# Kernel optimization log

Measured on AMD Instinct MI355X. Metric: run time of the kernel, lower is better.

## Reference

```python
import jax, jax.numpy as jnp
import numpy as np

D_MODEL = 256
N_HEADS = 8
HEAD_DIM = D_MODEL // N_HEADS  # 32
N_LEVELS = 4
N_POINTS = 4
LEVEL_SHAPES = [(100, 100), (50, 50), (25, 25), (13, 13)]
LEVEL_STARTS = [0] + list(np.cumsum([h * w for h, w in LEVEL_SHAPES]))[:-1]
LEN_IN = int(sum(h * w for h, w in LEVEL_SHAPES))  # 13294
BATCH = 2
LEN_Q = LEN_IN  # encoder self-attention


def _offset_bias():
    # faithful to MSDeformAttn._reset_parameters for sampling_offsets bias
    thetas = np.arange(N_HEADS, dtype=np.float32) * (2.0 * np.pi / N_HEADS)
    grid = np.stack([np.cos(thetas), np.sin(thetas)], -1)
    grid = grid / np.abs(grid).max(-1, keepdims=True)
    grid = np.tile(grid.reshape(N_HEADS, 1, 1, 2), (1, N_LEVELS, N_POINTS, 1))
    for i in range(N_POINTS):
        grid[:, :, i, :] *= i + 1
    return jnp.asarray(grid.reshape(-1), dtype=jnp.float32)


def setup_inputs() -> dict:
    key = jax.random.key(0)
    ks = jax.random.split(key, 10)
    s = 1.0 / np.sqrt(D_MODEL)
    inp = {
        "query": jax.random.normal(ks[0], (BATCH, LEN_Q, D_MODEL), jnp.float32),
        "reference_points": jax.random.uniform(ks[1], (BATCH, LEN_Q, N_LEVELS, 2), jnp.float32),
        "input_flatten": jax.random.normal(ks[2], (BATCH, LEN_IN, D_MODEL), jnp.float32),
        "input_spatial_shapes": jnp.asarray(LEVEL_SHAPES, dtype=jnp.int32),
        "W_value": jax.random.normal(ks[3], (D_MODEL, D_MODEL), jnp.float32) * s,
        "b_value": jnp.zeros((D_MODEL,), jnp.float32),
        "W_off": jax.random.normal(ks[4], (D_MODEL, N_HEADS * N_LEVELS * N_POINTS * 2), jnp.float32) * 0.01,
        "b_off": _offset_bias(),
        "W_attn": jax.random.normal(ks[5], (D_MODEL, N_HEADS * N_LEVELS * N_POINTS), jnp.float32) * 0.01,
        "b_attn": jnp.zeros((N_HEADS * N_LEVELS * N_POINTS,), jnp.float32),
        "W_out": jax.random.normal(ks[6], (D_MODEL, D_MODEL), jnp.float32) * s,
        "b_out": jnp.zeros((D_MODEL,), jnp.float32),
    }
    return inp


def _corner(v_t, ix, iy, h, w):
    # v_t: (n, M, h*w, D); ix/iy: (n, M, LqP) int32. Zero padding outside.
    valid = (ix >= 0) & (ix < w) & (iy >= 0) & (iy < h)
    idx = jnp.clip(iy, 0, h - 1) * w + jnp.clip(ix, 0, w - 1)
    g = jnp.take_along_axis(v_t, idx[..., None], axis=2)  # (n, M, LqP, D)
    return g * valid[..., None].astype(v_t.dtype)


def _ms_deform_attn(query, reference_points, input_flatten,
                    W_value, b_value, W_off, b_off, W_attn, b_attn, W_out, b_out):
    n, lq, _ = query.shape
    value = (input_flatten @ W_value + b_value).reshape(n, LEN_IN, N_HEADS, HEAD_DIM)
    offs = (query @ W_off + b_off).reshape(n, lq, N_HEADS, N_LEVELS, N_POINTS, 2)
    aw = jax.nn.softmax(
        (query @ W_attn + b_attn).reshape(n, lq, N_HEADS, N_LEVELS * N_POINTS), axis=-1
    ).reshape(n, lq, N_HEADS, N_LEVELS, N_POINTS)
    # offset_normalizer = (w, h) per level
    norm = jnp.asarray([[w, h] for h, w in LEVEL_SHAPES], dtype=query.dtype)
    loc = reference_points[:, :, None, :, None, :] + offs / norm[None, None, None, :, None, :]

    acc = jnp.zeros((n, N_HEADS, lq, HEAD_DIM), dtype=value.dtype)
    for l, (h, w) in enumerate(LEVEL_SHAPES):
        s0 = LEVEL_STARTS[l]
        v_t = jnp.transpose(value[:, s0:s0 + h * w], (0, 2, 1, 3))  # (n, M, hw, D)
        ll = loc[:, :, :, l]  # (n, lq, M, P, 2) in [0,1]
        # grid_sample bilinear, align_corners=False: pixel = coord*size - 0.5
        x = ll[..., 0] * w - 0.5
        y = ll[..., 1] * h - 0.5
        x0 = jnp.floor(x); y0 = jnp.floor(y)
        tx = x - x0; ty = y - y0
        ix0 = x0.astype(jnp.int32); iy0 = y0.astype(jnp.int32)
        flat = lambda a: jnp.transpose(a, (0, 2, 1, 3)).reshape(n, N_HEADS, lq * N_POINTS)
        ix0f, iy0f = flat(ix0), flat(iy0)
        txf = flat(tx)[..., None]; tyf = flat(ty)[..., None]
        g00 = _corner(v_t, ix0f, iy0f, h, w)
        g01 = _corner(v_t, ix0f + 1, iy0f, h, w)
        g10 = _corner(v_t, ix0f, iy0f + 1, h, w)
        g11 = _corner(v_t, ix0f + 1, iy0f + 1, h, w)
        samp = (g00 * (1 - txf) * (1 - tyf) + g01 * txf * (1 - tyf)
                + g10 * (1 - txf) * tyf + g11 * txf * tyf)
        samp = samp.reshape(n, N_HEADS, lq, N_POINTS, HEAD_DIM)
        wl = jnp.transpose(aw[:, :, :, l], (0, 2, 1, 3))[..., None]  # (n, M, lq, P, 1)
        acc = acc + (samp * wl).sum(axis=3)

    out = jnp.transpose(acc, (0, 2, 1, 3)).reshape(n, lq, D_MODEL)
    return out @ W_out + b_out


def reference(query, reference_points, input_flatten, input_spatial_shapes,
              W_value, b_value, W_off, b_off, W_attn, b_attn, W_out, b_out):
    # input_spatial_shapes carried for signature fidelity; level geometry is static.
    return _ms_deform_attn(query, reference_points, input_flatten,
                           W_value, b_value, W_off, b_off, W_attn, b_attn, W_out, b_out)
```

## Files before the change

kernel.cpp:

```cpp
#include <hip/hip_runtime.h>

#define NH 8
#define HD 32
#define NL 4
#define NP 4
#define DM 256
#define LEN_IN_C 13294
#define LQ_C 13294
#define B_C 2
#define M_TOTAL (B_C * LQ_C)
#define MT_TILES 1662

typedef __attribute__((ext_vector_type(8))) short short8;
typedef __attribute__((ext_vector_type(4))) float floatx4;
typedef __attribute__((ext_vector_type(2))) float floatx2;

__device__ __forceinline__ unsigned short f2bf(float x) {
    union { float f; unsigned int u; } a; a.f = x;
    unsigned int r = (a.u + 0x7FFFu + ((a.u >> 16) & 1u)) >> 16;
    return (unsigned short)r;
}
__device__ __forceinline__ floatx2 up2(unsigned int u) {
    union { unsigned int u; float f; } lo, hi;
    lo.u = u << 16; hi.u = u & 0xffff0000u;
    floatx2 r; r.x = lo.f; r.y = hi.f; return r;
}
__device__ __forceinline__ unsigned int cvtpk_bf16(float lo, float hi) {
    unsigned int r;
    asm("v_cvt_pk_bf16_f32 %0, %1, %2" : "=v"(r) : "v"(lo), "v"(hi));
    return r;
}

__device__ __forceinline__ void conv_b_body(const float* __restrict__ W,
                                            unsigned short* __restrict__ Bsw,
                                            int Nsrc, int NTsrc, int NTtotal, int ntOff,
                                            int vblk) {
    const int u = vblk * 256 + threadIdx.x;
    const int lane = u & 63;
    const int unit = u >> 6;
    const int ntl = unit % NTsrc;
    const int kc = unit / NTsrc;
    const int n = ntl * 16 + (lane & 15);
    const int k0 = kc * 32 + (lane >> 4) * 8;
    short8 v;
#pragma unroll
    for (int j = 0; j < 8; ++j)
        v[j] = (short)f2bf(W[(size_t)(k0 + j) * Nsrc + n]);
    ((short8*)Bsw)[(size_t)(kc * NTtotal + ntOff + ntl) * 64 + lane] = v;
}

__global__ __launch_bounds__(256) void conv_weights_kernel(const float* __restrict__ Wv,
                                                           const float* __restrict__ Woff,
                                                           const float* __restrict__ Wattn,
                                                           const float* __restrict__ Wout,
                                                           const float* __restrict__ boff,
                                                           const float* __restrict__ battn,
                                                           unsigned short* __restrict__ BswV,
                                                           unsigned short* __restrict__ BswOA,
                                                           unsigned short* __restrict__ BswO,
                                                           float* __restrict__ fbias,
                                                           unsigned short* __restrict__ value,
                                                           unsigned short* __restrict__ AccSw) {
    const int blk = blockIdx.x;
    if (blk < 32)        conv_b_body(Wv,    BswV,  256, 16, 16, 0,  blk);
    else if (blk < 64)   conv_b_body(Woff,  BswOA, 256, 16, 24, 0,  blk - 32);
    else if (blk < 80)   conv_b_body(Wattn, BswOA, 128,  8, 24, 16, blk - 64);
    else if (blk < 112)  conv_b_body(Wout,  BswO,  256, 16, 16, 0,  blk - 80);
    else if (blk < 114) {
        const int t = (blk - 112) * 256 + threadIdx.x;
        if (t < 384) fbias[t] = (t < 256) ? boff[t] : battn[t - 256];
        else if (t < 416) {
            const int j = t - 384;
            value[-32 + j] = 0;
            value[(size_t)M_TOTAL * 256 + j] = 0;
        }
    } else {
        const int idx = threadIdx.x;
        if (idx < 128) {
            const int kc = idx >> 4;
            const int sub = idx & 15;
            const int lane = (12 + (sub & 3)) + 16 * (sub >> 2);
            const size_t unit = (size_t)(1661 * 8 + kc) * 64 + lane;
            short8 z = (short8){0, 0, 0, 0, 0, 0, 0, 0};
            ((short8*)AccSw)[unit] = z;
        }
    }
}

template <int NT, int OUTMODE>
__global__ __launch_bounds__(256) void mfma_gemm_f32a(const float* __restrict__ A,
                                                      const unsigned short* __restrict__ Bsw,
                                                      const float* __restrict__ bias,
                                                      void* __restrict__ Cout, int M) {
    constexpr int NTW = NT / 4;
    const int tid = threadIdx.x;
    const int lane = tid & 63;
    const int wave = tid >> 6;
    const int rt0 = blockIdx.x * 2;
    const int m = lane & 15;
    const int q = lane >> 4;

    const float* Ar0 = A + (size_t)min(rt0 * 16 + m, M - 1) * 256 + q * 8;
    const float* Ar1 = A + (size_t)min(rt0 * 16 + 16 + m, M - 1) * 256 + q * 8;
    const short8* Bu = (const short8*)Bsw;

    floatx4 acc[2][NTW];
#pragma unroll
    for (int r = 0; r < 2; ++r)
#pragma unroll
        for (int t = 0; t < NTW; ++t) acc[r][t] = (floatx4){0.f, 0.f, 0.f, 0.f};

#pragma unroll 2
    for (int kc = 0; kc < 8; ++kc) {
        const float4 f00 = *(const float4*)(Ar0 + kc * 32);
        const float4 f01 = *(const float4*)(Ar0 + kc * 32 + 4);
        const float4 f10 = *(const float4*)(Ar1 + kc * 32);
        const float4 f11 = *(const float4*)(Ar1 + kc * 32 + 4);
        union { uint4 u; short8 s; } c0, c1;
        c0.u.x = cvtpk_bf16(f00.x, f00.y); c0.u.y = cvtpk_bf16(f00.z, f00.w);
        c0.u.z = cvtpk_bf16(f01.x, f01.y); c0.u.w = cvtpk_bf16(f01.z, f01.w);
        c1.u.x = cvtpk_bf16(f10.x, f10.y); c1.u.y = cvtpk_bf16(f10.z, f10.w);
        c1.u.z = cvtpk_bf16(f11.x, f11.y); c1.u.w = cvtpk_bf16(f11.z, f11.w);
        const short8 a0 = c0.s;
        const short8 a1 = c1.s;
#pragma unroll
        for (int t = 0; t < NTW; ++t) {
            const short8 b = Bu[(size_t)(kc * NT + wave * NTW + t) * 64 + lane];
            acc[0][t] = __builtin_amdgcn_mfma_f32_16x16x32_bf16(a0, b, acc[0][t], 0, 0, 0);
            acc[1][t] = __builtin_amdgcn_mfma_f32_16x16x32_bf16(a1, b, acc[1][t], 0, 0, 0);
        }
    }

    const int N = NT * 16;
    const int colq = lane & 15;
    const int rowq = (lane >> 4) * 4;
#pragma unroll
    for (int t = 0; t < NTW; ++t) {
        const int col = (wave * NTW + t) * 16 + colq;
        const float bc = bias[col];
#pragma unroll
        for (int r = 0; r < 2; ++r) {
            const int rowb = (rt0 + r) * 16 + rowq;
#pragma unroll
            for (int reg = 0; reg < 4; ++reg) {
                const int row = rowb + reg;
                if (row < M) {
                    const float v = acc[r][t][reg] + bc;
                    if (OUTMODE == 1) {
                        const int bb = row >= LEN_IN_C;
                        const int pos = row - (bb ? LEN_IN_C : 0);
                        const int hh = col >> 5;
                        const int dd = col & 31;
                        ((unsigned short*)Cout)[((size_t)((bb << 3) + hh) * LEN_IN_C + pos) * 32 + dd] = f2bf(v);
                    } else {
                        ((float*)Cout)[(size_t)row * N + col] = v;
                    }
                }
            }
        }
    }
}

template <int NT, bool OUT_BF16>
__global__ __launch_bounds__(256) void mfma_gemm_kernel(const unsigned short* __restrict__ Asw,
                                                        const unsigned short* __restrict__ Bsw,
                                                        const float* __restrict__ bias,
                                                        void* __restrict__ Cout, int M) {
    constexpr int NTW = NT / 4;
    const int tid = threadIdx.x;
    const int lane = tid & 63;
    const int wave = tid >> 6;
    const int rt0 = blockIdx.x * 2;

    const short8* Au = (const short8*)Asw;
    const short8* Bu = (const short8*)Bsw;

    floatx4 acc[2][NTW];
#pragma unroll
    for (int r = 0; r < 2; ++r)
#pragma unroll
        for (int t = 0; t < NTW; ++t) acc[r][t] = (floatx4){0.f, 0.f, 0.f, 0.f};

#pragma unroll 2
    for (int kc = 0; kc < 8; ++kc) {
        const short8 a0 = Au[(size_t)(rt0 * 8 + kc) * 64 + lane];
        const short8 a1 = Au[(size_t)((rt0 + 1) * 8 + kc) * 64 + lane];
#pragma unroll
        for (int t = 0; t < NTW; ++t) {
            const short8 b = Bu[(size_t)(kc * NT + wave * NTW + t) * 64 + lane];
            acc[0][t] = __builtin_amdgcn_mfma_f32_16x16x32_bf16(a0, b, acc[0][t], 0, 0, 0);
            acc[1][t] = __builtin_amdgcn_mfma_f32_16x16x32_bf16(a1, b, acc[1][t], 0, 0, 0);
        }
    }

    const int N = NT * 16;
    const int colq = lane & 15;
    const int rowq = (lane >> 4) * 4;
#pragma unroll
    for (int t = 0; t < NTW; ++t) {
        const int col = (wave * NTW + t) * 16 + colq;
        const float bc = bias[col];
#pragma unroll
        for (int r = 0; r < 2; ++r) {
            const int rowb = (rt0 + r) * 16 + rowq;
#pragma unroll
            for (int reg = 0; reg < 4; ++reg) {
                const int row = rowb + reg;
                if (row < M) {
                    const float v = acc[r][t][reg] + bc;
                    if (OUT_BF16)
                        ((unsigned short*)Cout)[(size_t)row * N + col] = f2bf(v);
                    else
                        ((float*)Cout)[(size_t)row * N + col] = v;
                }
            }
        }
    }
}

__global__ __launch_bounds__(256, 8) void msda_sample_kernel(const float* __restrict__ refp,
                                                             const unsigned short* __restrict__ value,
                                                             const float* __restrict__ fused,
                                                             unsigned short* __restrict__ AccSw) {
    constexpr int lvl_hw[4] = {100, 50, 25, 13};
    constexpr int lvl_s[4] = {0, 10000, 12500, 13125};

    const int bq0 = blockIdx.x * 4;
    const int tid = threadIdx.x;

    __shared__ float s_ref[32];
    __shared__ int2 s_pi[4 * 8 * 17];
    __shared__ float4 s_pw[4 * 8 * 17];

    if (tid < 32) s_ref[tid] = refp[(size_t)bq0 * 8 + tid];
    __syncthreads();

#pragma unroll
    for (int jj = 0; jj < 2; ++jj) {
        const int job = jj * 256 + tid;
        const int qq = job >> 7;
        const int t = job & 127;
        const int h = t >> 4;
        const int l = (t >> 2) & 3;
        const int bq = bq0 + qq;
        const int b = (bq >= LQ_C) ? 1 : 0;

        const float logit = fused[(size_t)bq * 384 + 256 + t];
        float m = logit;
#pragma unroll
        for (int mask = 1; mask < 16; mask <<= 1) m = fmaxf(m, __shfl_xor(m, mask));
        const float e = expf(logit - m);
        float s = e;
#pragma unroll
        for (int mask = 1; mask < 16; mask <<= 1) s += __shfl_xor(s, mask);
        const float aw = e / s;

        const int whl = lvl_hw[l];
        const float fwh = (float)whl;
        const float2 oxy = *(const float2*)(fused + (size_t)bq * 384 + t * 2);
        const float x = s_ref[qq * 8 + l * 2] * fwh + oxy.x - 0.5f;
        const float y = s_ref[qq * 8 + l * 2 + 1] * fwh + oxy.y - 0.5f;
        const float x0f = floorf(x), y0f = floorf(y);
        const float tx = x - x0f, ty = y - y0f;
        const int ix0 = (int)x0f, iy0 = (int)y0f;

        const bool xv0 = (unsigned)ix0 < (unsigned)whl;
        const bool xv1 = (unsigned)(ix0 + 1) < (unsigned)whl;
        const bool yv0 = (unsigned)iy0 < (unsigned)whl;
        const bool yv1 = (unsigned)(iy0 + 1) < (unsigned)whl;

        const int cxp = min(max(ix0, -1), whl - 1);
        const int cy0 = min(max(iy0, 0), whl - 1);
        const int cy1 = min(max(iy0 + 1, 0), whl - 1);

        const int posb = (b * 8 + h) * LEN_IN_C + lvl_s[l];
        int2 aa;
        aa.x = (posb + cy0 * whl + cxp) * 64;
        aa.y = (posb + cy1 * whl + cxp) * 64;
        float4 wv;
        wv.x = (xv0 && yv0) ? aw * (1.f - tx) * (1.f - ty) : 0.f;
        wv.y = (xv1 && yv0) ? aw * tx * (1.f - ty) : 0.f;
        wv.z = (xv0 && yv1) ? aw * (1.f - tx) * ty : 0.f;
        wv.w = (xv1 && yv1) ? aw * tx * ty : 0.f;
        const int slot = (qq * 8 + h) * 17 + (t & 15);
        s_pi[slot] = aa;
        s_pw[slot] = wv;
    }
    __syncthreads();

    const int qq = tid >> 6;
    const int h = (tid >> 3) & 7;
    const int l8 = tid & 7;
    const char* vbp = (const char*)value + l8 * 16;
    const int pbase = (qq * 8 + h) * 17;
    const bool right = (l8 & 4) != 0;

    floatx2 acc0 = (floatx2){0.f, 0.f}, acc1 = acc0, acc2 = acc0, acc3 = acc0;
#pragma unroll 2
    for (int pt = 0; pt < 16; ++pt) {
        const int2 aa = s_pi[pbase + pt];
        const float4 wv = s_pw[pbase + pt];
        const float wt = right ? wv.y : wv.x;
        const float wb = right ? wv.w : wv.z;
        const uint4 vt = *(const uint4*)(vbp + aa.x);
        const uint4 vbm = *(const uint4*)(vbp + aa.y);
        const floatx2 w2t = (floatx2){wt, wt};
        const floatx2 w2b = (floatx2){wb, wb};
        acc0 += w2t * up2(vt.x);
        acc1 += w2t * up2(vt.y);
        acc2 += w2t * up2(vt.z);
        acc3 += w2t * up2(vt.w);
        acc0 += w2b * up2(vbm.x);
        acc1 += w2b * up2(vbm.y);
        acc2 += w2b * up2(vbm.z);
        acc3 += w2b * up2(vbm.w);
    }

    float r0 = acc0.x, r1 = acc0.y, r2 = acc1.x, r3 = acc1.y;
    float r4 = acc2.x, r5 = acc2.y, r6 = acc3.x, r7 = acc3.y;
    r0 += __shfl_xor(r0, 4); r1 += __shfl_xor(r1, 4);
    r2 += __shfl_xor(r2, 4); r3 += __shfl_xor(r3, 4);
    r4 += __shfl_xor(r4, 4); r5 += __shfl_xor(r5, 4);
    r6 += __shfl_xor(r6, 4); r7 += __shfl_xor(r7, 4);

    if (!right) {
        const int bq = bq0 + qq;
        const int rt = bq >> 4, mm = bq & 15;
        const int unit = (rt * 8 + h) * 64 + ((l8 & 3) * 16 + mm);
        uint4 o;
        o.x = cvtpk_bf16(r0, r1);
        o.y = cvtpk_bf16(r2, r3);
        o.z = cvtpk_bf16(r4, r5);
        o.w = cvtpk_bf16(r6, r7);
        *(uint4*)(AccSw + (size_t)unit * 8) = o;
    }
}

extern "C" void kernel_launch(void* const* d_in, const int* in_sizes, int n_in,
                              void* d_out, int out_size, void* d_ws, size_t ws_size,
                              hipStream_t stream) {
    const float* query  = (const float*)d_in[0];
    const float* refp   = (const float*)d_in[1];
    const float* inflat = (const float*)d_in[2];
    const float* Wv    = (const float*)d_in[4];
    const float* bv    = (const float*)d_in[5];
    const float* Woff  = (const float*)d_in[6];
    const float* boff  = (const float*)d_in[7];
    const float* Wattn = (const float*)d_in[8];
    const float* battn = (const float*)d_in[9];
    const float* Wout  = (const float*)d_in[10];
    const float* bout  = (const float*)d_in[11];
    float* out = (float*)d_out;

    char* p = (char*)d_ws;
    unsigned short* AccSw = (unsigned short*)p;
    p += (size_t)MT_TILES * 8 * 64 * 8 * sizeof(unsigned short);
    unsigned short* BswV = (unsigned short*)p;   p += (size_t)8 * 16 * 64 * 8 * 2;
    unsigned short* BswOA = (unsigned short*)p;  p += (size_t)8 * 24 * 64 * 8 * 2;
    unsigned short* BswO = (unsigned short*)p;   p += (size_t)8 * 16 * 64 * 8 * 2;
    float* fbias = (float*)p;                    p += 384 * sizeof(float);
    unsigned short* value = (unsigned short*)p + 32;
    p += ((size_t)M_TOTAL * 256 + 64) * sizeof(unsigned short);
    float* fused = (float*)p;                    p += (size_t)M_TOTAL * 384 * 4;

    const int M = M_TOTAL;
    const int gemmBlocks = MT_TILES / 2;

    conv_weights_kernel<<<115, 256, 0, stream>>>(Wv, Woff, Wattn, Wout, boff, battn,
                                                 BswV, BswOA, BswO, fbias, value, AccSw);
    mfma_gemm_f32a<16, 1><<<gemmBlocks, 256, 0, stream>>>(inflat, BswV, bv, value, M);
    mfma_gemm_f32a<24, 0><<<gemmBlocks, 256, 0, stream>>>(query, BswOA, fbias, fused, M);
    msda_sample_kernel<<<M / 4, 256, 0, stream>>>(refp, value, fused, AccSw);
    mfma_gemm_kernel<16, false><<<gemmBlocks, 256, 0, stream>>>(AccSw, BswO, bout, out, M);
}
```

Measured before the change: 226.1 us.

## Merge front GEMMs into one launch, shrink GEMM tiles, regroup sampling by head

```diff
diff --git a/kernel.cpp b/kernel.cpp
--- a/kernel.cpp
+++ b/kernel.cpp
@@ -10,6 +10,8 @@
 #define B_C 2
 #define M_TOTAL (B_C * LQ_C)
 #define MT_TILES 1662
+#define GQ 32
+#define QBLKS 831
 
 typedef __attribute__((ext_vector_type(8))) short short8;
 typedef __attribute__((ext_vector_type(4))) float floatx4;
@@ -88,46 +90,36 @@
 }
 
 template <int NT, int OUTMODE>
-__global__ __launch_bounds__(256) void mfma_gemm_f32a(const float* __restrict__ A,
-                                                      const unsigned short* __restrict__ Bsw,
-                                                      const float* __restrict__ bias,
-                                                      void* __restrict__ Cout, int M) {
+__device__ __forceinline__ void gemm_f32a_body(const float* __restrict__ A,
+                                               const unsigned short* __restrict__ Bsw,
+                                               const float* __restrict__ bias,
+                                               void* __restrict__ Cout, int M, int rt) {
     constexpr int NTW = NT / 4;
     const int tid = threadIdx.x;
     const int lane = tid & 63;
     const int wave = tid >> 6;
-    const int rt0 = blockIdx.x * 2;
     const int m = lane & 15;
     const int q = lane >> 4;
 
-    const float* Ar0 = A + (size_t)min(rt0 * 16 + m, M - 1) * 256 + q * 8;
-    const float* Ar1 = A + (size_t)min(rt0 * 16 + 16 + m, M - 1) * 256 + q * 8;
+    const float* Ar = A + (size_t)min(rt * 16 + m, M - 1) * 256 + q * 8;
     const short8* Bu = (const short8*)Bsw;
 
-    floatx4 acc[2][NTW];
-#pragma unroll
-    for (int r = 0; r < 2; ++r)
-#pragma unroll
-        for (int t = 0; t < NTW; ++t) acc[r][t] = (floatx4){0.f, 0.f, 0.f, 0.f};
+    floatx4 acc[NTW];
+#pragma unroll
+    for (int t = 0; t < NTW; ++t) acc[t] = (floatx4){0.f, 0.f, 0.f, 0.f};
 
 #pragma unroll 2
     for (int kc = 0; kc < 8; ++kc) {
-        const float4 f00 = *(const float4*)(Ar0 + kc * 32);
-        const float4 f01 = *(const float4*)(Ar0 + kc * 32 + 4);
-        const float4 f10 = *(const float4*)(Ar1 + kc * 32);
-        const float4 f11 = *(const float4*)(Ar1 + kc * 32 + 4);
-        union { uint4 u; short8 s; } c0, c1;
-        c0.u.x = cvtpk_bf16(f00.x, f00.y); c0.u.y = cvtpk_bf16(f00.z, f00.w);
-        c0.u.z = cvtpk_bf16(f01.x, f01.y); c0.u.w = cvtpk_bf16(f01.z, f01.w);
-        c1.u.x = cvtpk_bf16(f10.x, f10.y); c1.u.y = cvtpk_bf16(f10.z, f10.w);
-        c1.u.z = cvtpk_bf16(f11.x, f11.y); c1.u.w = cvtpk_bf16(f11.z, f11.w);
-        const short8 a0 = c0.s;
-        const short8 a1 = c1.s;
+        const float4 f0 = *(const float4*)(Ar + kc * 32);
+        const float4 f1 = *(const float4*)(Ar + kc * 32 + 4);
+        union { uint4 u; short8 s; } c;
+        c.u.x = cvtpk_bf16(f0.x, f0.y); c.u.y = cvtpk_bf16(f0.z, f0.w);
+        c.u.z = cvtpk_bf16(f1.x, f1.y); c.u.w = cvtpk_bf16(f1.z, f1.w);
+        const short8 a = c.s;
 #pragma unroll
         for (int t = 0; t < NTW; ++t) {
             const short8 b = Bu[(size_t)(kc * NT + wave * NTW + t) * 64 + lane];
-            acc[0][t] = __builtin_amdgcn_mfma_f32_16x16x32_bf16(a0, b, acc[0][t], 0, 0, 0);
-            acc[1][t] = __builtin_amdgcn_mfma_f32_16x16x32_bf16(a1, b, acc[1][t], 0, 0, 0);
+            acc[t] = __builtin_amdgcn_mfma_f32_16x16x32_bf16(a, b, acc[t], 0, 0, 0);
         }
     }
 
@@ -139,61 +131,68 @@
         const int col = (wave * NTW + t) * 16 + colq;
         const float bc = bias[col];
 #pragma unroll
-        for (int r = 0; r < 2; ++r) {
-            const int rowb = (rt0 + r) * 16 + rowq;
-#pragma unroll
-            for (int reg = 0; reg < 4; ++reg) {
-                const int row = rowb + reg;
-                if (row < M) {
-                    const float v = acc[r][t][reg] + bc;
-                    if (OUTMODE == 1) {
-                        const int bb = row >= LEN_IN_C;
-                        const int pos = row - (bb ? LEN_IN_C : 0);
-                        const int hh = col >> 5;
-                        const int dd = col & 31;
-                        ((unsigned short*)Cout)[((size_t)((bb << 3) + hh) * LEN_IN_C + pos) * 32 + dd] = f2bf(v);
-                    } else {
-                        ((float*)Cout)[(size_t)row * N + col] = v;
-                    }
+        for (int reg = 0; reg < 4; ++reg) {
+            const int row = rt * 16 + rowq + reg;
+            if (row < M) {
+                const float v = acc[t][reg] + bc;
+                if (OUTMODE == 1) {
+                    const int bb = row >= LEN_IN_C;
+                    const int pos = row - (bb ? LEN_IN_C : 0);
+                    const int hh = col >> 5;
+                    const int dd = col & 31;
+                    ((unsigned short*)Cout)[((size_t)((bb << 3) + hh) * LEN_IN_C + pos) * 32 + dd] = f2bf(v);
+                } else {
+                    ((float*)Cout)[(size_t)row * N + col] = v;
                 }
             }
         }
     }
 }
 
-template <int NT, bool OUT_BF16>
-__global__ __launch_bounds__(256) void mfma_gemm_kernel(const unsigned short* __restrict__ Asw,
+__global__ __launch_bounds__(256) void front_gemm_kernel(const float* __restrict__ inflat,
+                                                         const float* __restrict__ query,
+                                                         const unsigned short* __restrict__ BswV,
+                                                         const unsigned short* __restrict__ BswOA,
+                                                         const float* __restrict__ bv,
+                                                         const float* __restrict__ fbias,
+                                                         unsigned short* __restrict__ value,
+                                                         float* __restrict__ fused, int M) {
+    const int x = blockIdx.x;
+    const int rt = x >> 1;
+    if ((x & 1) == 0)
+        gemm_f32a_body<16, 1>(inflat, BswV, bv, (void*)value, M, rt);
+    else
+        gemm_f32a_body<24, 0>(query, BswOA, fbias, (void*)fused, M, rt);
+}
+
+__global__ __launch_bounds__(256) void back_gemm_kernel(const unsigned short* __restrict__ Asw,
                                                         const unsigned short* __restrict__ Bsw,
                                                         const float* __restrict__ bias,
-                                                        void* __restrict__ Cout, int M) {
-    constexpr int NTW = NT / 4;
+                                                        float* __restrict__ Cout, int M) {
+    constexpr int NT = 16;
+    constexpr int NTW = 4;
     const int tid = threadIdx.x;
     const int lane = tid & 63;
     const int wave = tid >> 6;
-    const int rt0 = blockIdx.x * 2;
+    const int rt = blockIdx.x;
 
     const short8* Au = (const short8*)Asw;
     const short8* Bu = (const short8*)Bsw;
 
-    floatx4 acc[2][NTW];
-#pragma unroll
-    for (int r = 0; r < 2; ++r)
-#pragma unroll
-        for (int t = 0; t < NTW; ++t) acc[r][t] = (floatx4){0.f, 0.f, 0.f, 0.f};
+    floatx4 acc[NTW];
+#pragma unroll
+    for (int t = 0; t < NTW; ++t) acc[t] = (floatx4){0.f, 0.f, 0.f, 0.f};
 
 #pragma unroll 2
     for (int kc = 0; kc < 8; ++kc) {
-        const short8 a0 = Au[(size_t)(rt0 * 8 + kc) * 64 + lane];
-        const short8 a1 = Au[(size_t)((rt0 + 1) * 8 + kc) * 64 + lane];
+        const short8 a = Au[(size_t)(rt * 8 + kc) * 64 + lane];
 #pragma unroll
         for (int t = 0; t < NTW; ++t) {
             const short8 b = Bu[(size_t)(kc * NT + wave * NTW + t) * 64 + lane];
-            acc[0][t] = __builtin_amdgcn_mfma_f32_16x16x32_bf16(a0, b, acc[0][t], 0, 0, 0);
-            acc[1][t] = __builtin_amdgcn_mfma_f32_16x16x32_bf16(a1, b, acc[1][t], 0, 0, 0);
-        }
-    }
-
-    const int N = NT * 16;
+            acc[t] = __builtin_amdgcn_mfma_f32_16x16x32_bf16(a, b, acc[t], 0, 0, 0);
+        }
+    }
+
     const int colq = lane & 15;
     const int rowq = (lane >> 4) * 4;
 #pragma unroll
@@ -201,19 +200,10 @@
         const int col = (wave * NTW + t) * 16 + colq;
         const float bc = bias[col];
 #pragma unroll
-        for (int r = 0; r < 2; ++r) {
-            const int rowb = (rt0 + r) * 16 + rowq;
-#pragma unroll
-            for (int reg = 0; reg < 4; ++reg) {
-                const int row = rowb + reg;
-                if (row < M) {
-                    const float v = acc[r][t][reg] + bc;
-                    if (OUT_BF16)
-                        ((unsigned short*)Cout)[(size_t)row * N + col] = f2bf(v);
-                    else
-                        ((float*)Cout)[(size_t)row * N + col] = v;
-                }
-            }
+        for (int reg = 0; reg < 4; ++reg) {
+            const int row = rt * 16 + rowq + reg;
+            if (row < M)
+                Cout[(size_t)row * 256 + col] = acc[t][reg] + bc;
         }
     }
 }
@@ -225,27 +215,28 @@
     constexpr int lvl_hw[4] = {100, 50, 25, 13};
     constexpr int lvl_s[4] = {0, 10000, 12500, 13125};
 
-    const int bq0 = blockIdx.x * 4;
+    const int wg = blockIdx.x;
+    const int h = wg & 7;
+    const int q0 = (wg >> 3) * GQ;
     const int tid = threadIdx.x;
 
-    __shared__ float s_ref[32];
-    __shared__ int2 s_pi[4 * 8 * 17];
-    __shared__ float4 s_pw[4 * 8 * 17];
-
-    if (tid < 32) s_ref[tid] = refp[(size_t)bq0 * 8 + tid];
+    __shared__ float s_ref[GQ * 8];
+    __shared__ int2 s_pi[GQ * 17];
+    __shared__ float4 s_pw[GQ * 17];
+
+    s_ref[tid] = refp[min(q0 * 8 + tid, M_TOTAL * 8 - 1)];
     __syncthreads();
 
 #pragma unroll
     for (int jj = 0; jj < 2; ++jj) {
         const int job = jj * 256 + tid;
-        const int qq = job >> 7;
-        const int t = job & 127;
-        const int h = t >> 4;
-        const int l = (t >> 2) & 3;
-        const int bq = bq0 + qq;
+        const int qq = job >> 4;
+        const int t16 = job & 15;
+        const int l = t16 >> 2;
+        const int bq = min(q0 + qq, M_TOTAL - 1);
         const int b = (bq >= LQ_C) ? 1 : 0;
 
-        const float logit = fused[(size_t)bq * 384 + 256 + t];
+        const float logit = fused[(size_t)bq * 384 + 256 + h * 16 + t16];
         float m = logit;
 #pragma unroll
         for (int mask = 1; mask < 16; mask <<= 1) m = fmaxf(m, __shfl_xor(m, mask));
@@ -257,7 +248,7 @@
 
         const int whl = lvl_hw[l];
         const float fwh = (float)whl;
-        const float2 oxy = *(const float2*)(fused + (size_t)bq * 384 + t * 2);
+        const float2 oxy = *(const float2*)(fused + (size_t)bq * 384 + (h * 16 + t16) * 2);
         const float x = s_ref[qq * 8 + l * 2] * fwh + oxy.x - 0.5f;
         const float y = s_ref[qq * 8 + l * 2 + 1] * fwh + oxy.y - 0.5f;
         const float x0f = floorf(x), y0f = floorf(y);
@@ -282,17 +273,16 @@
         wv.y = (xv1 && yv0) ? aw * tx * (1.f - ty) : 0.f;
         wv.z = (xv0 && yv1) ? aw * (1.f - tx) * ty : 0.f;
         wv.w = (xv1 && yv1) ? aw * tx * ty : 0.f;
-        const int slot = (qq * 8 + h) * 17 + (t & 15);
+        const int slot = qq * 17 + t16;
         s_pi[slot] = aa;
         s_pw[slot] = wv;
     }
     __syncthreads();
 
-    const int qq = tid >> 6;
-    const int h = (tid >> 3) & 7;
+    const int qq = tid >> 3;
     const int l8 = tid & 7;
     const char* vbp = (const char*)value + l8 * 16;
-    const int pbase = (qq * 8 + h) * 17;
+    const int pbase = qq * 17;
     const bool right = (l8 & 4) != 0;
 
     floatx2 acc0 = (floatx2){0.f, 0.f}, acc1 = acc0, acc2 = acc0, acc3 = acc0;
@@ -323,8 +313,8 @@
     r4 += __shfl_xor(r4, 4); r5 += __shfl_xor(r5, 4);
     r6 += __shfl_xor(r6, 4); r7 += __shfl_xor(r7, 4);
 
-    if (!right) {
-        const int bq = bq0 + qq;
+    const int bq = q0 + qq;
+    if (!right && bq < M_TOTAL) {
         const int rt = bq >> 4, mm = bq & 15;
         const int unit = (rt * 8 + h) * 64 + ((l8 & 3) * 16 + mm);
         uint4 o;
@@ -364,12 +354,11 @@
     float* fused = (float*)p;                    p += (size_t)M_TOTAL * 384 * 4;
 
     const int M = M_TOTAL;
-    const int gemmBlocks = MT_TILES / 2;
 
     conv_weights_kernel<<<115, 256, 0, stream>>>(Wv, Woff, Wattn, Wout, boff, battn,
                                                  BswV, BswOA, BswO, fbias, value, AccSw);
-    mfma_gemm_f32a<16, 1><<<gemmBlocks, 256, 0, stream>>>(inflat, BswV, bv, value, M);
-    mfma_gemm_f32a<24, 0><<<gemmBlocks, 256, 0, stream>>>(query, BswOA, fbias, fused, M);
-    msda_sample_kernel<<<M / 4, 256, 0, stream>>>(refp, value, fused, AccSw);
-    mfma_gemm_kernel<16, false><<<gemmBlocks, 256, 0, stream>>>(AccSw, BswO, bout, out, M);
-}
+    front_gemm_kernel<<<MT_TILES * 2, 256, 0, stream>>>(inflat, query, BswV, BswOA,
+                                                        bv, fbias, value, fused, M);
+    msda_sample_kernel<<<QBLKS * 8, 256, 0, stream>>>(refp, value, fused, AccSw);
+    back_gemm_kernel<<<MT_TILES, 256, 0, stream>>>(AccSw, BswO, bout, out, M);
+}
```

Result: no change. 221.8 us (-1.9%).
